# Performance work log

Measured on AMD Instinct MI355X. Metric: run time of the kernel, lower is better.

Reference implementation:

```python
import jax, jax.numpy as jnp
import numpy as np

INPUT_SIZE = 13
HIDDEN = 128
SEQ = 30
BATCH = 32768
OUT = 128
BN_EPS = 1e-5


def _lstm_layer(x, Wih, Whh, bih, bhh):
    """Single LSTM layer, batch_first. x: [B,T,I]. PyTorch gate order i,f,g,o."""
    B = x.shape[0]
    H = Whh.shape[1]
    # Precompute input contribution for all timesteps as one big GEMM: [B,T,4H]
    xg = jnp.einsum('bti,gi->btg', x, Wih) + bih + bhh

    def step(carry, xt):
        h, c = carry
        g = xt + h @ Whh.T  # [B,4H]
        i, f, gg, o = jnp.split(g, 4, axis=-1)
        i = jax.nn.sigmoid(i)
        f = jax.nn.sigmoid(f)
        o = jax.nn.sigmoid(o)
        c = f * c + i * jnp.tanh(gg)
        h = o * jnp.tanh(c)
        return (h, c), h

    h0 = jnp.zeros((B, H), dtype=x.dtype)
    c0 = jnp.zeros((B, H), dtype=x.dtype)
    _, hs = jax.lax.scan(step, (h0, c0), jnp.swapaxes(xg, 0, 1))  # hs: [T,B,H]
    return jnp.swapaxes(hs, 0, 1)  # [B,T,H]


def setup_inputs() -> dict:
    key = jax.random.key(0)
    ks = jax.random.split(key, 12)

    def xavier(k, shape):
        fan_out, fan_in = shape[0], shape[1]
        bound = float(np.sqrt(6.0 / (fan_in + fan_out)))
        return jax.random.uniform(k, shape, jnp.float32, -bound, bound)

    return {
        'x': jax.random.normal(ks[0], (BATCH, SEQ, INPUT_SIZE), jnp.float32),
        'Wih0': xavier(ks[1], (4 * HIDDEN, INPUT_SIZE)),
        'Whh0': xavier(ks[2], (4 * HIDDEN, HIDDEN)),
        'bih0': jnp.zeros((4 * HIDDEN,), jnp.float32),
        'bhh0': jnp.zeros((4 * HIDDEN,), jnp.float32),
        'Wih1': xavier(ks[3], (4 * HIDDEN, HIDDEN)),
        'Whh1': xavier(ks[4], (4 * HIDDEN, HIDDEN)),
        'bih1': jnp.zeros((4 * HIDDEN,), jnp.float32),
        'bhh1': jnp.zeros((4 * HIDDEN,), jnp.float32),
        'fcW': xavier(ks[5], (OUT, HIDDEN)),
        'fcb': jnp.zeros((OUT,), jnp.float32),
        'gamma': jnp.ones((OUT,), jnp.float32),
        'beta': jnp.zeros((OUT,), jnp.float32),
    }


def reference(x, Wih0, Whh0, bih0, bhh0, Wih1, Whh1, bih1, bhh1, fcW, fcb, gamma, beta):
    # 2-layer LSTM (inter-layer dropout is identity in eval mode)
    h1 = _lstm_layer(x, Wih0, Whh0, bih0, bhh0)
    h2 = _lstm_layer(h1, Wih1, Whh1, bih1, bhh1)
    last = h2[:, -1, :]  # [B,H] (dropout(0.5) is identity in eval)
    y = last @ fcW.T + fcb  # [B,OUT]
    # BatchNorm1d (training-mode forward: biased batch statistics)
    mean = jnp.mean(y, axis=0)
    var = jnp.var(y, axis=0)
    return gamma * (y - mean) * jax.lax.rsqrt(var + BN_EPS) + beta
```

## Files before the change

### kernel.cpp

```cpp
#include <hip/hip_runtime.h>

#define BATCH 32768
#define SEQ 30
#define INP 13
#define HID 128
#define ROWS 16
#define NBLK (BATCH/ROWS)
#define THREADS 512
#define H1PITCH 136
#define H1SLOT (ROWS*H1PITCH)

#define LDS_WIH1 65536
#define LDS_H1   (LDS_WIH1)
#define LDS_H2   (LDS_WIH1 + 2*H1SLOT)
#define LDS_SHORTS (LDS_WIH1 + 4*H1SLOT)
#define LDS_BYTES (LDS_SHORTS*2)

typedef float f32x4  __attribute__((ext_vector_type(4)));
typedef short bf16x8 __attribute__((ext_vector_type(8)));

__device__ inline unsigned short f2bf(float f){
  unsigned int u = __float_as_uint(f);
  u = u + 0x7fffu + ((u >> 16) & 1u);
  return (unsigned short)(u >> 16);
}
__device__ inline float exp2_hw(float x){ float r; asm("v_exp_f32 %0, %1" : "=v"(r) : "v"(x)); return r; }
__device__ inline float rcp_hw (float x){ float r; asm("v_rcp_f32 %0, %1" : "=v"(r) : "v"(x)); return r; }
__device__ inline float sigm (float x){ return rcp_hw(1.f + exp2_hw(-1.4426950408889634f*x)); }
__device__ inline float tanh_(float x){ return 1.f - 2.f*rcp_hw(1.f + exp2_hw(2.8853900817779268f*x)); }

__global__ void conv_frag(const float* __restrict__ src, unsigned short* __restrict__ dst,
                          int gates, int K, int nks){
  int tid = blockIdx.x*256 + threadIdx.x;
  int total = gates*8*nks*64;
  if(tid >= total) return;
  int lane = tid & 63; int rest = tid >> 6;
  int ks = rest % nks; rest /= nks;
  int ct = rest & 7;   int g  = rest >> 3;
  int lr = lane & 15, lg = lane >> 4;
  int row = g*128 + ct*16 + lr;
  unsigned short out[8];
  #pragma unroll
  for(int e=0;e<8;e++){
    int k = ks*32 + lg*8 + e;
    float v = (k<K) ? src[(long)row*K + k] : 0.f;
    out[e] = f2bf(v);
  }
  *(uint4*)(dst + (long)tid*8) = *(const uint4*)out;
}

__global__ void conv_bias(const float* __restrict__ bih0, const float* __restrict__ bhh0,
                          const float* __restrict__ bih1, const float* __restrict__ bhh1,
                          float* __restrict__ dst){
  int i = blockIdx.x*256 + threadIdx.x;
  if(i < 512)       dst[i] = bih0[i] + bhh0[i];
  else if(i < 1024) dst[i] = bih1[i-512] + bhh1[i-512];
}

__global__ __launch_bounds__(256)
void stage_x(const float* __restrict__ x, unsigned short* __restrict__ xf){
  __shared__ float xt[ROWS*SEQ*INP];
  const int blk = blockIdx.x, tid = threadIdx.x;
  for(int i=tid; i<ROWS*SEQ*INP; i+=256) xt[i] = x[(long)blk*ROWS*SEQ*INP + i];
  __syncthreads();
  for(int j=tid; j<SEQ*64; j+=256){
    int t = j>>6, lane = j&63, lr = lane&15, lg = lane>>4;
    unsigned short out[8];
    #pragma unroll
    for(int e=0;e<8;e++){
      int k = lg*8+e;
      float v = (k<INP) ? xt[lr*(SEQ*INP) + t*INP + k] : 0.f;
      out[e] = f2bf(v);
    }
    *(uint4*)(xf + (((long)t*NBLK + blk)*64 + lane)*8) = *(const uint4*)out;
  }
}

__global__ __launch_bounds__(THREADS, 2)
void lstm_pipe(const unsigned short* __restrict__ xf,
               const unsigned short* __restrict__ whh0f, const unsigned short* __restrict__ wih0f,
               const unsigned short* __restrict__ wih1f, const unsigned short* __restrict__ whh1f,
               const unsigned short* __restrict__ fcf,   const float* __restrict__ biases,
               const float* __restrict__ fcb,
               float* __restrict__ y, float* __restrict__ partial)
{
  extern __shared__ unsigned short lds[];
  unsigned short* wihs = lds;
  unsigned short* h1r  = lds + LDS_H1;
  unsigned short* h2r  = lds + LDS_H2;

  const int tid=threadIdx.x, lane=tid&63, wv=tid>>6, lr=lane&15, lg=lane>>4;
  const int blk=blockIdx.x, row0=blk*ROWS, myc=wv*16+lr;

  {
    const uint4* src4 = (const uint4*)wih1f;
    uint4* dst4 = (uint4*)lds;
    #pragma unroll
    for(int i=0;i<16;++i) dst4[tid + i*THREADS] = src4[tid + i*THREADS];
  }

  bf16x8 w0h[4][4], w1h[4][4], w0i[4];
  float bias0[4], bias1[4];
  #pragma unroll
  for(int g=0; g<4; ++g){
    #pragma unroll
    for(int ks=0; ks<4; ++ks){
      long off = (long)((((g*8+wv)*4+ks)*64+lane))*8;
      w0h[g][ks] = *(const bf16x8*)(whh0f + off);
      w1h[g][ks] = *(const bf16x8*)(whh1f + off);
    }
    w0i[g] = *(const bf16x8*)(wih0f + (long)(((g*8+wv)*64+lane))*8);
    bias0[g] = biases[g*HID+myc];
    bias1[g] = biases[512 + g*HID+myc];
  }
  float c1[4]={0,0,0,0}, c2[4]={0,0,0,0};
  __syncthreads();

  f32x4 acc1[4];
  for(int tau=0; tau<=SEQ; ++tau){
    const int s_prev = (tau-1)&1;
    bf16x8 ax;
    if(tau<SEQ) ax = *(const bf16x8*)(xf + (((long)tau*NBLK + blk)*64 + lane)*8);
    bf16x8 a1[4];
    if(tau>=1){
      #pragma unroll
      for(int ks=0;ks<4;++ks)
        a1[ks] = *(const bf16x8*)(h1r + s_prev*H1SLOT + lr*H1PITCH + ks*32 + lg*8);
    }
    if(tau>=1){
      #pragma unroll
      for(int g=0;g<4;++g) acc1[g]=(f32x4){bias1[g],bias1[g],bias1[g],bias1[g]};
      #pragma unroll
      for(int ks=0;ks<4;++ks){
        #pragma unroll
        for(int g=0;g<4;++g){
          bf16x8 wf = *(const bf16x8*)(wihs + (long)((((g*8+wv)*4+ks)*64+lane))*8);
          acc1[g]=__builtin_amdgcn_mfma_f32_16x16x32_bf16(a1[ks],wf,acc1[g],0,0,0);
        }
      }
      if(tau>=2){
        #pragma unroll
        for(int ks=0;ks<4;++ks){
          bf16x8 a2 = *(const bf16x8*)(h2r + (tau&1)*H1SLOT + lr*H1PITCH + ks*32 + lg*8);
          #pragma unroll
          for(int g=0;g<4;++g)
            acc1[g]=__builtin_amdgcn_mfma_f32_16x16x32_bf16(a2,w1h[g][ks],acc1[g],0,0,0);
        }
      }
    }
    f32x4 acc0[4];
    if(tau<SEQ){
      #pragma unroll
      for(int g=0;g<4;++g){
        acc0[g]=(f32x4){bias0[g],bias0[g],bias0[g],bias0[g]};
        acc0[g]=__builtin_amdgcn_mfma_f32_16x16x32_bf16(ax,w0i[g],acc0[g],0,0,0);
      }
      if(tau>=1){
        #pragma unroll
        for(int ks=0;ks<4;++ks)
          #pragma unroll
          for(int g=0;g<4;++g)
            acc0[g]=__builtin_amdgcn_mfma_f32_16x16x32_bf16(a1[ks],w0h[g][ks],acc0[g],0,0,0);
      }
    }
    if(tau<SEQ){
      #pragma unroll
      for(int r=0;r<4;++r){
        float iv=sigm(acc0[0][r]), fv=sigm(acc0[1][r]), gv=tanh_(acc0[2][r]), ov=sigm(acc0[3][r]);
        c1[r]=fv*c1[r]+iv*gv;
        h1r[(tau&1)*H1SLOT + (lg*4+r)*H1PITCH + myc] = f2bf(ov*tanh_(c1[r]));
      }
    }
    if(tau>=1){
      #pragma unroll
      for(int r=0;r<4;++r){
        float iv=sigm(acc1[0][r]), fv=sigm(acc1[1][r]), gv=tanh_(acc1[2][r]), ov=sigm(acc1[3][r]);
        c2[r]=fv*c2[r]+iv*gv;
        h2r[s_prev*H1SLOT + (lg*4+r)*H1PITCH + myc] = f2bf(ov*tanh_(c2[r]));
      }
    }
    __syncthreads();
  }

  f32x4 ay=(f32x4){fcb[myc],fcb[myc],fcb[myc],fcb[myc]};
  #pragma unroll
  for(int ks=0;ks<4;++ks){
    bf16x8 bfc = *(const bf16x8*)(fcf + (long)(((wv*4+ks)*64+lane))*8);
    bf16x8 a2  = *(const bf16x8*)(h2r + 1*H1SLOT + lr*H1PITCH + ks*32 + lg*8);
    ay=__builtin_amdgcn_mfma_f32_16x16x32_bf16(a2,bfc,ay,0,0,0);
  }
  float s=0.f, sq=0.f;
  #pragma unroll
  for(int r=0;r<4;++r){
    float v=ay[r];
    y[(long)(row0+lg*4+r)*HID+myc]=v;
    s+=v; sq+=v*v;
  }
  s +=__shfl_xor(s ,16,64); s +=__shfl_xor(s ,32,64);
  sq+=__shfl_xor(sq,16,64); sq+=__shfl_xor(sq,32,64);
  if(lg==0){
    partial[(long)myc      *NBLK+blk]=s;
    partial[(long)(HID+myc)*NBLK+blk]=sq;
  }
}

__global__ void bn_reduce(const float* __restrict__ partial, float* __restrict__ mv){
  int c=blockIdx.x;
  float s=0.f,sq=0.f;
  for(int i=threadIdx.x;i<NBLK;i+=256){
    s +=partial[(long)c      *NBLK+i];
    sq+=partial[(long)(HID+c)*NBLK+i];
  }
  #pragma unroll
  for(int m=32;m>=1;m>>=1){ s+=__shfl_xor(s,m,64); sq+=__shfl_xor(sq,m,64); }
  __shared__ float rs[4],rq[4];
  int w=threadIdx.x>>6;
  if((threadIdx.x&63)==0){ rs[w]=s; rq[w]=sq; }
  __syncthreads();
  if(threadIdx.x==0){
    s=rs[0]+rs[1]+rs[2]+rs[3]; sq=rq[0]+rq[1]+rq[2]+rq[3];
    float mean=s/(float)BATCH;
    float var=sq/(float)BATCH-mean*mean;
    mv[c]=mean; mv[HID+c]=rsqrtf(var+1e-5f);
  }
}

__global__ void bn_apply(float* __restrict__ y, const float* __restrict__ mv,
                         const float* __restrict__ gamma, const float* __restrict__ beta){
  long idx=((long)blockIdx.x*256+threadIdx.x)*4;
  int c=(int)(idx&(HID-1));
  float4 v=*reinterpret_cast<float4*>(y+idx);
  v.x=gamma[c+0]*(v.x-mv[c+0])*mv[HID+c+0]+beta[c+0];
  v.y=gamma[c+1]*(v.y-mv[c+1])*mv[HID+c+1]+beta[c+1];
  v.z=gamma[c+2]*(v.z-mv[c+2])*mv[HID+c+2]+beta[c+2];
  v.w=gamma[c+3]*(v.w-mv[c+3])*mv[HID+c+3]+beta[c+3];
  *reinterpret_cast<float4*>(y+idx)=v;
}

extern "C" void kernel_launch(void* const* d_in, const int* in_sizes, int n_in,
                              void* d_out, int out_size, void* d_ws, size_t ws_size,
                              hipStream_t stream){
  const float* x    =(const float*)d_in[0];
  const float* Wih0 =(const float*)d_in[1];
  const float* Whh0 =(const float*)d_in[2];
  const float* bih0 =(const float*)d_in[3];
  const float* bhh0 =(const float*)d_in[4];
  const float* Wih1 =(const float*)d_in[5];
  const float* Whh1 =(const float*)d_in[6];
  const float* bih1 =(const float*)d_in[7];
  const float* bhh1 =(const float*)d_in[8];
  const float* fcW  =(const float*)d_in[9];
  const float* fcb  =(const float*)d_in[10];
  const float* gamma=(const float*)d_in[11];
  const float* beta =(const float*)d_in[12];
  float* y=(float*)d_out;

  char* ws = (char*)d_ws;
  const long XF_BYTES = (long)SEQ*NBLK*64*8*2;
  unsigned short* xf    = (unsigned short*)(ws + 0);
  unsigned short* whh0f = (unsigned short*)(ws + XF_BYTES);
  unsigned short* wih0f = (unsigned short*)(ws + XF_BYTES + 131072);
  unsigned short* wih1f = (unsigned short*)(ws + XF_BYTES + 163840);
  unsigned short* whh1f = (unsigned short*)(ws + XF_BYTES + 294912);
  unsigned short* fcf   = (unsigned short*)(ws + XF_BYTES + 425984);
  float*          biases= (float*)         (ws + XF_BYTES + 458752);
  float*          partial=(float*)         (ws + XF_BYTES + 462848);
  float*          mv    = partial + (long)2*HID*NBLK;

  conv_frag<<<32,256,0,stream>>>(Whh0, whh0f, 4, HID, 4);
  conv_frag<<<8, 256,0,stream>>>(Wih0, wih0f, 4, INP, 1);
  conv_frag<<<32,256,0,stream>>>(Wih1, wih1f, 4, HID, 4);
  conv_frag<<<32,256,0,stream>>>(Whh1, whh1f, 4, HID, 4);
  conv_frag<<<8, 256,0,stream>>>(fcW,  fcf,   1, HID, 4);
  conv_bias<<<4, 256,0,stream>>>(bih0,bhh0,bih1,bhh1,biases);
  stage_x<<<NBLK,256,0,stream>>>(x, xf);

  hipFuncSetAttribute((const void*)lstm_pipe,
                      hipFuncAttributeMaxDynamicSharedMemorySize, LDS_BYTES);
  lstm_pipe<<<NBLK,THREADS,LDS_BYTES,stream>>>(
      xf, whh0f, wih0f, wih1f, whh1f, fcf, biases, fcb, y, partial);
  bn_reduce<<<HID,256,0,stream>>>(partial,mv);
  bn_apply<<<(BATCH*HID)/(256*4),256,0,stream>>>(y,mv,gamma,beta);
}
```

Baseline: 543.9 us.

## Split LSTM layers across separate wave groups with swizzled LDS ring

Doubles the block to 1024 threads so waves 0-7 compute layer 0 and waves 8-15 compute layer 1 of the wavefront-pipelined recurrence, rather than each wave doing both layers. Each wave now holds only one recurrent weight set in registers, which cuts register pressure, and the two layers' MFMA and activation work can interleave across waves. The padded h buffers are replaced by an XOR-swizzled ring in LDS to avoid bank conflicts. In exchange, more waves per block contend on the same barrier each step, and occupancy depends on how many 1024-thread blocks fit per CU.

```diff
diff --git a/kernel.cpp b/kernel.cpp
--- a/kernel.cpp
+++ b/kernel.cpp
@@ -6,14 +6,11 @@
 #define HID 128
 #define ROWS 16
 #define NBLK (BATCH/ROWS)
-#define THREADS 512
-#define H1PITCH 136
-#define H1SLOT (ROWS*H1PITCH)
-
-#define LDS_WIH1 65536
-#define LDS_H1   (LDS_WIH1)
-#define LDS_H2   (LDS_WIH1 + 2*H1SLOT)
-#define LDS_SHORTS (LDS_WIH1 + 4*H1SLOT)
+#define THREADS 1024
+
+#define LDS_WIHS 65536
+#define LDS_RING (LDS_WIHS)
+#define LDS_SHORTS (LDS_WIHS + 4*2048)
 #define LDS_BYTES (LDS_SHORTS*2)
 
 typedef float f32x4  __attribute__((ext_vector_type(4)));
@@ -28,6 +25,13 @@
 __device__ inline float rcp_hw (float x){ float r; asm("v_rcp_f32 %0, %1" : "=v"(r) : "v"(x)); return r; }
 __device__ inline float sigm (float x){ return rcp_hw(1.f + exp2_hw(-1.4426950408889634f*x)); }
 __device__ inline float tanh_(float x){ return 1.f - 2.f*rcp_hw(1.f + exp2_hw(2.8853900817779268f*x)); }
+
+__device__ inline int ring_rd(int slot, int row, int kshort){
+  return slot*2048 + row*128 + (kshort ^ (row<<3));
+}
+__device__ inline int ring_wr(int slot, int row, int col){
+  return slot*2048 + row*128 + (col ^ (row<<3));
+}
 
 __global__ void conv_frag(const float* __restrict__ src, unsigned short* __restrict__ dst,
                           int gates, int K, int nks){
@@ -76,131 +80,125 @@
   }
 }
 
-__global__ __launch_bounds__(THREADS, 2)
-void lstm_pipe(const unsigned short* __restrict__ xf,
-               const unsigned short* __restrict__ whh0f, const unsigned short* __restrict__ wih0f,
-               const unsigned short* __restrict__ wih1f, const unsigned short* __restrict__ whh1f,
-               const unsigned short* __restrict__ fcf,   const float* __restrict__ biases,
-               const float* __restrict__ fcb,
-               float* __restrict__ y, float* __restrict__ partial)
+__global__ __launch_bounds__(THREADS, 4)
+void lstm_split(const unsigned short* __restrict__ xf,
+                const unsigned short* __restrict__ whh0f, const unsigned short* __restrict__ wih0f,
+                const unsigned short* __restrict__ wih1f, const unsigned short* __restrict__ whh1f,
+                const unsigned short* __restrict__ fcf,   const float* __restrict__ biases,
+                const float* __restrict__ fcb,
+                float* __restrict__ y, float* __restrict__ partial)
 {
   extern __shared__ unsigned short lds[];
   unsigned short* wihs = lds;
-  unsigned short* h1r  = lds + LDS_H1;
-  unsigned short* h2r  = lds + LDS_H2;
+  unsigned short* ring = lds + LDS_RING;
 
   const int tid=threadIdx.x, lane=tid&63, wv=tid>>6, lr=lane&15, lg=lane>>4;
-  const int blk=blockIdx.x, row0=blk*ROWS, myc=wv*16+lr;
+  const bool isL0 = (wv < 8);
+  const int ct = isL0 ? wv : (wv-8);
+  const int myc = ct*16 + lr;
+  const int blk=blockIdx.x, row0=blk*ROWS;
 
   {
     const uint4* src4 = (const uint4*)wih1f;
     uint4* dst4 = (uint4*)lds;
     #pragma unroll
-    for(int i=0;i<16;++i) dst4[tid + i*THREADS] = src4[tid + i*THREADS];
-  }
-
-  bf16x8 w0h[4][4], w1h[4][4], w0i[4];
-  float bias0[4], bias1[4];
+    for(int i=0;i<8;++i) dst4[tid + i*THREADS] = src4[tid + i*THREADS];
+  }
+
+  bf16x8 wh[4][4], w0i[4];
+  float bias[4];
+  const unsigned short* whf = isL0 ? whh0f : whh1f;
   #pragma unroll
   for(int g=0; g<4; ++g){
     #pragma unroll
-    for(int ks=0; ks<4; ++ks){
-      long off = (long)((((g*8+wv)*4+ks)*64+lane))*8;
-      w0h[g][ks] = *(const bf16x8*)(whh0f + off);
-      w1h[g][ks] = *(const bf16x8*)(whh1f + off);
-    }
-    w0i[g] = *(const bf16x8*)(wih0f + (long)(((g*8+wv)*64+lane))*8);
-    bias0[g] = biases[g*HID+myc];
-    bias1[g] = biases[512 + g*HID+myc];
-  }
-  float c1[4]={0,0,0,0}, c2[4]={0,0,0,0};
+    for(int ks=0; ks<4; ++ks)
+      wh[g][ks] = *(const bf16x8*)(whf + (long)((((g*8+ct)*4+ks)*64+lane))*8);
+    if(isL0) w0i[g] = *(const bf16x8*)(wih0f + (long)(((g*8+ct)*64+lane))*8);
+    bias[g] = biases[(isL0?0:512) + g*HID + myc];
+  }
+  float c[4] = {0,0,0,0};
   __syncthreads();
 
-  f32x4 acc1[4];
   for(int tau=0; tau<=SEQ; ++tau){
-    const int s_prev = (tau-1)&1;
-    bf16x8 ax;
-    if(tau<SEQ) ax = *(const bf16x8*)(xf + (((long)tau*NBLK + blk)*64 + lane)*8);
-    bf16x8 a1[4];
-    if(tau>=1){
-      #pragma unroll
-      for(int ks=0;ks<4;++ks)
-        a1[ks] = *(const bf16x8*)(h1r + s_prev*H1SLOT + lr*H1PITCH + ks*32 + lg*8);
-    }
-    if(tau>=1){
-      #pragma unroll
-      for(int g=0;g<4;++g) acc1[g]=(f32x4){bias1[g],bias1[g],bias1[g],bias1[g]};
-      #pragma unroll
-      for(int ks=0;ks<4;++ks){
+    if(isL0){
+      if(tau<SEQ){
+        bf16x8 ax = *(const bf16x8*)(xf + (((long)tau*NBLK + blk)*64 + lane)*8);
+        f32x4 acc[4];
         #pragma unroll
         for(int g=0;g<4;++g){
-          bf16x8 wf = *(const bf16x8*)(wihs + (long)((((g*8+wv)*4+ks)*64+lane))*8);
-          acc1[g]=__builtin_amdgcn_mfma_f32_16x16x32_bf16(a1[ks],wf,acc1[g],0,0,0);
+          acc[g]=(f32x4){bias[g],bias[g],bias[g],bias[g]};
+          acc[g]=__builtin_amdgcn_mfma_f32_16x16x32_bf16(ax, w0i[g], acc[g],0,0,0);
+        }
+        if(tau>=1){
+          const int s1=(tau-1)&1;
+          #pragma unroll
+          for(int ks=0;ks<4;++ks){
+            bf16x8 a1 = *(const bf16x8*)(ring + ring_rd(s1, lr, ks*32+lg*8));
+            #pragma unroll
+            for(int g=0;g<4;++g)
+              acc[g]=__builtin_amdgcn_mfma_f32_16x16x32_bf16(a1, wh[g][ks], acc[g],0,0,0);
+          }
+        }
+        #pragma unroll
+        for(int r=0;r<4;++r){
+          float iv=sigm(acc[0][r]), fv=sigm(acc[1][r]), gv=tanh_(acc[2][r]), ov=sigm(acc[3][r]);
+          c[r]=fv*c[r]+iv*gv;
+          ring[ring_wr(tau&1, lg*4+r, myc)] = f2bf(ov*tanh_(c[r]));
         }
       }
-      if(tau>=2){
+    } else {
+      if(tau>=1){
+        f32x4 acc[4];
+        #pragma unroll
+        for(int g=0;g<4;++g) acc[g]=(f32x4){bias[g],bias[g],bias[g],bias[g]};
+        const int s1=(tau-1)&1, s2=2+(tau&1);
         #pragma unroll
         for(int ks=0;ks<4;++ks){
-          bf16x8 a2 = *(const bf16x8*)(h2r + (tau&1)*H1SLOT + lr*H1PITCH + ks*32 + lg*8);
+          bf16x8 a1 = *(const bf16x8*)(ring + ring_rd(s1, lr, ks*32+lg*8));
           #pragma unroll
-          for(int g=0;g<4;++g)
-            acc1[g]=__builtin_amdgcn_mfma_f32_16x16x32_bf16(a2,w1h[g][ks],acc1[g],0,0,0);
+          for(int g=0;g<4;++g){
+            bf16x8 wf = *(const bf16x8*)(wihs + (long)((((g*8+ct)*4+ks)*64+lane))*8);
+            acc[g]=__builtin_amdgcn_mfma_f32_16x16x32_bf16(a1, wf, acc[g],0,0,0);
+          }
+          if(tau>=2){
+            bf16x8 a2 = *(const bf16x8*)(ring + ring_rd(s2, lr, ks*32+lg*8));
+            #pragma unroll
+            for(int g=0;g<4;++g)
+              acc[g]=__builtin_amdgcn_mfma_f32_16x16x32_bf16(a2, wh[g][ks], acc[g],0,0,0);
+          }
+        }
+        #pragma unroll
+        for(int r=0;r<4;++r){
+          float iv=sigm(acc[0][r]), fv=sigm(acc[1][r]), gv=tanh_(acc[2][r]), ov=sigm(acc[3][r]);
+          c[r]=fv*c[r]+iv*gv;
+          ring[ring_wr(2+((tau-1)&1), lg*4+r, myc)] = f2bf(ov*tanh_(c[r]));
         }
       }
     }
-    f32x4 acc0[4];
-    if(tau<SEQ){
-      #pragma unroll
-      for(int g=0;g<4;++g){
-        acc0[g]=(f32x4){bias0[g],bias0[g],bias0[g],bias0[g]};
-        acc0[g]=__builtin_amdgcn_mfma_f32_16x16x32_bf16(ax,w0i[g],acc0[g],0,0,0);
-      }
-      if(tau>=1){
-        #pragma unroll
-        for(int ks=0;ks<4;++ks)
-          #pragma unroll
-          for(int g=0;g<4;++g)
-            acc0[g]=__builtin_amdgcn_mfma_f32_16x16x32_bf16(a1[ks],w0h[g][ks],acc0[g],0,0,0);
-      }
-    }
-    if(tau<SEQ){
-      #pragma unroll
-      for(int r=0;r<4;++r){
-        float iv=sigm(acc0[0][r]), fv=sigm(acc0[1][r]), gv=tanh_(acc0[2][r]), ov=sigm(acc0[3][r]);
-        c1[r]=fv*c1[r]+iv*gv;
-        h1r[(tau&1)*H1SLOT + (lg*4+r)*H1PITCH + myc] = f2bf(ov*tanh_(c1[r]));
-      }
-    }
-    if(tau>=1){
-      #pragma unroll
-      for(int r=0;r<4;++r){
-        float iv=sigm(acc1[0][r]), fv=sigm(acc1[1][r]), gv=tanh_(acc1[2][r]), ov=sigm(acc1[3][r]);
-        c2[r]=fv*c2[r]+iv*gv;
-        h2r[s_prev*H1SLOT + (lg*4+r)*H1PITCH + myc] = f2bf(ov*tanh_(c2[r]));
-      }
-    }
     __syncthreads();
   }
 
-  f32x4 ay=(f32x4){fcb[myc],fcb[myc],fcb[myc],fcb[myc]};
-  #pragma unroll
-  for(int ks=0;ks<4;++ks){
-    bf16x8 bfc = *(const bf16x8*)(fcf + (long)(((wv*4+ks)*64+lane))*8);
-    bf16x8 a2  = *(const bf16x8*)(h2r + 1*H1SLOT + lr*H1PITCH + ks*32 + lg*8);
-    ay=__builtin_amdgcn_mfma_f32_16x16x32_bf16(a2,bfc,ay,0,0,0);
-  }
-  float s=0.f, sq=0.f;
-  #pragma unroll
-  for(int r=0;r<4;++r){
-    float v=ay[r];
-    y[(long)(row0+lg*4+r)*HID+myc]=v;
-    s+=v; sq+=v*v;
-  }
-  s +=__shfl_xor(s ,16,64); s +=__shfl_xor(s ,32,64);
-  sq+=__shfl_xor(sq,16,64); sq+=__shfl_xor(sq,32,64);
-  if(lg==0){
-    partial[(long)myc      *NBLK+blk]=s;
-    partial[(long)(HID+myc)*NBLK+blk]=sq;
+  if(isL0){
+    f32x4 ay=(f32x4){fcb[myc],fcb[myc],fcb[myc],fcb[myc]};
+    #pragma unroll
+    for(int ks=0;ks<4;++ks){
+      bf16x8 bfc = *(const bf16x8*)(fcf + (long)(((ct*4+ks)*64+lane))*8);
+      bf16x8 a2  = *(const bf16x8*)(ring + ring_rd(3, lr, ks*32+lg*8));
+      ay=__builtin_amdgcn_mfma_f32_16x16x32_bf16(a2, bfc, ay,0,0,0);
+    }
+    float s=0.f, sq=0.f;
+    #pragma unroll
+    for(int r=0;r<4;++r){
+      float v=ay[r];
+      y[(long)(row0+lg*4+r)*HID+myc]=v;
+      s+=v; sq+=v*v;
+    }
+    s +=__shfl_xor(s ,16,64); s +=__shfl_xor(s ,32,64);
+    sq+=__shfl_xor(sq,16,64); sq+=__shfl_xor(sq,32,64);
+    if(lg==0){
+      partial[(long)myc      *NBLK+blk]=s;
+      partial[(long)(HID+myc)*NBLK+blk]=sq;
+    }
   }
 }
 
@@ -275,9 +273,9 @@
   conv_bias<<<4, 256,0,stream>>>(bih0,bhh0,bih1,bhh1,biases);
   stage_x<<<NBLK,256,0,stream>>>(x, xf);
 
-  hipFuncSetAttribute((const void*)lstm_pipe,
+  hipFuncSetAttribute((const void*)lstm_split,
                       hipFuncAttributeMaxDynamicSharedMemorySize, LDS_BYTES);
-  lstm_pipe<<<NBLK,THREADS,LDS_BYTES,stream>>>(
+  lstm_split<<<NBLK,THREADS,LDS_BYTES,stream>>>(
       xf, whh0f, wih0f, wih1f, whh1f, fcf, biases, fcb, y, partial);
   bn_reduce<<<HID,256,0,stream>>>(partial,mv);
   bn_apply<<<(BATCH*HID)/(256*4),256,0,stream>>>(y,mv,gamma,beta);
```

After: 1.031 ms. 89.6% more time.

## Make LSTM kernel persistent over row groups with swizzled LDS ring and x prefetch

Applied to the files above, without the earlier changes.

The main kernel now launches a fixed grid of 256 blocks, each looping over 8 row groups, so the per-block weight loads (Wih1 into LDS and the recurrent weights into registers) are paid once per block instead of once per 16-row group. The hidden-state staging buffers switch from padded pitch rows to an XOR-swizzled unpadded ring, to avoid LDS bank conflicts with a smaller footprint. The next timestep's x fragment is also prefetched one step ahead. The trade-off is fewer blocks in flight (256 blocks on a GPU with many CUs at 2 blocks per CU), which may leave CUs idle or hurt latency hiding.

```diff
diff --git a/kernel.cpp b/kernel.cpp
--- a/kernel.cpp
+++ b/kernel.cpp
@@ -6,14 +6,13 @@
 #define HID 128
 #define ROWS 16
 #define NBLK (BATCH/ROWS)
+#define GRID 256
+#define GPB (NBLK/GRID)
 #define THREADS 512
-#define H1PITCH 136
-#define H1SLOT (ROWS*H1PITCH)
-
-#define LDS_WIH1 65536
-#define LDS_H1   (LDS_WIH1)
-#define LDS_H2   (LDS_WIH1 + 2*H1SLOT)
-#define LDS_SHORTS (LDS_WIH1 + 4*H1SLOT)
+
+#define LDS_WIHS 65536
+#define LDS_RING (LDS_WIHS)
+#define LDS_SHORTS (LDS_WIHS + 4*2048)
 #define LDS_BYTES (LDS_SHORTS*2)
 
 typedef float f32x4  __attribute__((ext_vector_type(4)));
@@ -28,6 +27,13 @@
 __device__ inline float rcp_hw (float x){ float r; asm("v_rcp_f32 %0, %1" : "=v"(r) : "v"(x)); return r; }
 __device__ inline float sigm (float x){ return rcp_hw(1.f + exp2_hw(-1.4426950408889634f*x)); }
 __device__ inline float tanh_(float x){ return 1.f - 2.f*rcp_hw(1.f + exp2_hw(2.8853900817779268f*x)); }
+
+__device__ inline int ring_rd(int slot, int row, int kshort){
+  return slot*2048 + row*128 + (kshort ^ (row<<3));
+}
+__device__ inline int ring_wr(int slot, int row, int col){
+  return slot*2048 + row*128 + (col ^ (row<<3));
+}
 
 __global__ void conv_frag(const float* __restrict__ src, unsigned short* __restrict__ dst,
                           int gates, int K, int nks){
@@ -86,11 +92,10 @@
 {
   extern __shared__ unsigned short lds[];
   unsigned short* wihs = lds;
-  unsigned short* h1r  = lds + LDS_H1;
-  unsigned short* h2r  = lds + LDS_H2;
+  unsigned short* ring = lds + LDS_RING;
 
   const int tid=threadIdx.x, lane=tid&63, wv=tid>>6, lr=lane&15, lg=lane>>4;
-  const int blk=blockIdx.x, row0=blk*ROWS, myc=wv*16+lr;
+  const int myc = wv*16 + lr;
 
   {
     const uint4* src4 = (const uint4*)wih1f;
@@ -113,94 +118,104 @@
     bias0[g] = biases[g*HID+myc];
     bias1[g] = biases[512 + g*HID+myc];
   }
-  float c1[4]={0,0,0,0}, c2[4]={0,0,0,0};
   __syncthreads();
 
-  f32x4 acc1[4];
-  for(int tau=0; tau<=SEQ; ++tau){
-    const int s_prev = (tau-1)&1;
-    bf16x8 ax;
-    if(tau<SEQ) ax = *(const bf16x8*)(xf + (((long)tau*NBLK + blk)*64 + lane)*8);
-    bf16x8 a1[4];
-    if(tau>=1){
-      #pragma unroll
-      for(int ks=0;ks<4;++ks)
-        a1[ks] = *(const bf16x8*)(h1r + s_prev*H1SLOT + lr*H1PITCH + ks*32 + lg*8);
-    }
-    if(tau>=1){
-      #pragma unroll
-      for(int g=0;g<4;++g) acc1[g]=(f32x4){bias1[g],bias1[g],bias1[g],bias1[g]};
+  for(int grp=0; grp<GPB; ++grp){
+    const int blk  = blockIdx.x*GPB + grp;
+    const int row0 = blk*ROWS;
+    float c1[4]={0,0,0,0}, c2[4]={0,0,0,0};
+    f32x4 acc1[4];
+    bf16x8 ax = *(const bf16x8*)(xf + ((long)blk*64 + lane)*8);
+
+    for(int tau=0; tau<=SEQ; ++tau){
+      const int s_prev = (tau-1)&1;
+      const int tnext = (tau+1 < SEQ) ? (tau+1) : (SEQ-1);
+      bf16x8 ax_n = *(const bf16x8*)(xf + (((long)tnext*NBLK + blk)*64 + lane)*8);
+      bf16x8 a1[4];
+      if(tau>=1){
+        #pragma unroll
+        for(int ks=0;ks<4;++ks)
+          a1[ks] = *(const bf16x8*)(ring + ring_rd(s_prev, lr, ks*32+lg*8));
+      }
+      if(tau>=1){
+        #pragma unroll
+        for(int g=0;g<4;++g) acc1[g]=(f32x4){bias1[g],bias1[g],bias1[g],bias1[g]};
+        #pragma unroll
+        for(int ks=0;ks<4;++ks){
+          #pragma unroll
+          for(int g=0;g<4;++g){
+            bf16x8 wf = *(const bf16x8*)(wihs + (long)((((g*8+wv)*4+ks)*64+lane))*8);
+            acc1[g]=__builtin_amdgcn_mfma_f32_16x16x32_bf16(a1[ks],wf,acc1[g],0,0,0);
+          }
+        }
+        if(tau>=2){
+          #pragma unroll
+          for(int ks=0;ks<4;++ks){
+            bf16x8 a2 = *(const bf16x8*)(ring + ring_rd(2+(tau&1), lr, ks*32+lg*8));
+            #pragma unroll
+            for(int g=0;g<4;++g)
+              acc1[g]=__builtin_amdgcn_mfma_f32_16x16x32_bf16(a2,w1h[g][ks],acc1[g],0,0,0);
+          }
+        }
+      }
+      f32x4 acc0[4];
+      if(tau<SEQ){
+        #pragma unroll
+        for(int g=0;g<4;++g){
+          acc0[g]=(f32x4){bias0[g],bias0[g],bias0[g],bias0[g]};
+          acc0[g]=__builtin_amdgcn_mfma_f32_16x16x32_bf16(ax,w0i[g],acc0[g],0,0,0);
+        }
+        if(tau>=1){
+          #pragma unroll
+          for(int ks=0;ks<4;++ks)
+            #pragma unroll
+            for(int g=0;g<4;++g)
+              acc0[g]=__builtin_amdgcn_mfma_f32_16x16x32_bf16(a1[ks],w0h[g][ks],acc0[g],0,0,0);
+        }
+      }
+      if(tau<SEQ){
+        #pragma unroll
+        for(int r=0;r<4;++r){
+          float iv=sigm(acc0[0][r]), fv=sigm(acc0[1][r]), gv=tanh_(acc0[2][r]), ov=sigm(acc0[3][r]);
+          c1[r]=fv*c1[r]+iv*gv;
+          ring[ring_wr(tau&1, lg*4+r, myc)] = f2bf(ov*tanh_(c1[r]));
+        }
+      }
+      if(tau>=1){
+        #pragma unroll
+        for(int r=0;r<4;++r){
+          float iv=sigm(acc1[0][r]), fv=sigm(acc1[1][r]), gv=tanh_(acc1[2][r]), ov=sigm(acc1[3][r]);
+          c2[r]=fv*c2[r]+iv*gv;
+          ring[ring_wr(2+s_prev, lg*4+r, myc)] = f2bf(ov*tanh_(c2[r]));
+        }
+      }
+      ax = ax_n;
+      __syncthreads();
+    }
+
+    {
+      f32x4 ay=(f32x4){fcb[myc],fcb[myc],fcb[myc],fcb[myc]};
       #pragma unroll
       for(int ks=0;ks<4;++ks){
-        #pragma unroll
-        for(int g=0;g<4;++g){
-          bf16x8 wf = *(const bf16x8*)(wihs + (long)((((g*8+wv)*4+ks)*64+lane))*8);
-          acc1[g]=__builtin_amdgcn_mfma_f32_16x16x32_bf16(a1[ks],wf,acc1[g],0,0,0);
-        }
-      }
-      if(tau>=2){
-        #pragma unroll
-        for(int ks=0;ks<4;++ks){
-          bf16x8 a2 = *(const bf16x8*)(h2r + (tau&1)*H1SLOT + lr*H1PITCH + ks*32 + lg*8);
-          #pragma unroll
-          for(int g=0;g<4;++g)
-            acc1[g]=__builtin_amdgcn_mfma_f32_16x16x32_bf16(a2,w1h[g][ks],acc1[g],0,0,0);
-        }
-      }
-    }
-    f32x4 acc0[4];
-    if(tau<SEQ){
-      #pragma unroll
-      for(int g=0;g<4;++g){
-        acc0[g]=(f32x4){bias0[g],bias0[g],bias0[g],bias0[g]};
-        acc0[g]=__builtin_amdgcn_mfma_f32_16x16x32_bf16(ax,w0i[g],acc0[g],0,0,0);
-      }
-      if(tau>=1){
-        #pragma unroll
-        for(int ks=0;ks<4;++ks)
-          #pragma unroll
-          for(int g=0;g<4;++g)
-            acc0[g]=__builtin_amdgcn_mfma_f32_16x16x32_bf16(a1[ks],w0h[g][ks],acc0[g],0,0,0);
-      }
-    }
-    if(tau<SEQ){
+        bf16x8 bfc = *(const bf16x8*)(fcf + (long)(((wv*4+ks)*64+lane))*8);
+        bf16x8 a2  = *(const bf16x8*)(ring + ring_rd(3, lr, ks*32+lg*8));
+        ay=__builtin_amdgcn_mfma_f32_16x16x32_bf16(a2,bfc,ay,0,0,0);
+      }
+      float s=0.f, sq=0.f;
       #pragma unroll
       for(int r=0;r<4;++r){
-        float iv=sigm(acc0[0][r]), fv=sigm(acc0[1][r]), gv=tanh_(acc0[2][r]), ov=sigm(acc0[3][r]);
-        c1[r]=fv*c1[r]+iv*gv;
-        h1r[(tau&1)*H1SLOT + (lg*4+r)*H1PITCH + myc] = f2bf(ov*tanh_(c1[r]));
-      }
-    }
-    if(tau>=1){
-      #pragma unroll
-      for(int r=0;r<4;++r){
-        float iv=sigm(acc1[0][r]), fv=sigm(acc1[1][r]), gv=tanh_(acc1[2][r]), ov=sigm(acc1[3][r]);
-        c2[r]=fv*c2[r]+iv*gv;
-        h2r[s_prev*H1SLOT + (lg*4+r)*H1PITCH + myc] = f2bf(ov*tanh_(c2[r]));
+        float v=ay[r];
+        y[(long)(row0+lg*4+r)*HID+myc]=v;
+        s+=v; sq+=v*v;
+      }
+      s +=__shfl_xor(s ,16,64); s +=__shfl_xor(s ,32,64);
+      sq+=__shfl_xor(sq,16,64); sq+=__shfl_xor(sq,32,64);
+      if(lg==0){
+        partial[(long)myc      *NBLK+blk]=s;
+        partial[(long)(HID+myc)*NBLK+blk]=sq;
       }
     }
     __syncthreads();
-  }
-
-  f32x4 ay=(f32x4){fcb[myc],fcb[myc],fcb[myc],fcb[myc]};
-  #pragma unroll
-  for(int ks=0;ks<4;++ks){
-    bf16x8 bfc = *(const bf16x8*)(fcf + (long)(((wv*4+ks)*64+lane))*8);
-    bf16x8 a2  = *(const bf16x8*)(h2r + 1*H1SLOT + lr*H1PITCH + ks*32 + lg*8);
-    ay=__builtin_amdgcn_mfma_f32_16x16x32_bf16(a2,bfc,ay,0,0,0);
-  }
-  float s=0.f, sq=0.f;
-  #pragma unroll
-  for(int r=0;r<4;++r){
-    float v=ay[r];
-    y[(long)(row0+lg*4+r)*HID+myc]=v;
-    s+=v; sq+=v*v;
-  }
-  s +=__shfl_xor(s ,16,64); s +=__shfl_xor(s ,32,64);
-  sq+=__shfl_xor(sq,16,64); sq+=__shfl_xor(sq,32,64);
-  if(lg==0){
-    partial[(long)myc      *NBLK+blk]=s;
-    partial[(long)(HID+myc)*NBLK+blk]=sq;
   }
 }
 
@@ -277,7 +292,7 @@
 
   hipFuncSetAttribute((const void*)lstm_pipe,
                       hipFuncAttributeMaxDynamicSharedMemorySize, LDS_BYTES);
-  lstm_pipe<<<NBLK,THREADS,LDS_BYTES,stream>>>(
+  lstm_pipe<<<GRID,THREADS,LDS_BYTES,stream>>>(
       xf, whh0f, wih0f, wih1f, whh1f, fcf, biases, fcb, y, partial);
   bn_reduce<<<HID,256,0,stream>>>(partial,mv);
   bn_apply<<<(BATCH*HID)/(256*4),256,0,stream>>>(y,mv,gamma,beta);
```

Measured after the change: 618.2 us. 13.6% more time.
